# Kernel tuning notes

Hardware: AMD Instinct MI355X
Metric: run time of the kernel (lower is better)

Reference implementation:

```python
import jax, jax.numpy as jnp
import numpy as np
import math

B, T, D, H = 2, 2048, 1024, 16
DH = D // H


def setup_inputs() -> dict:
    key = jax.random.key(0)
    k1, k2, k3 = jax.random.split(key, 3)
    scale_in = 1.0 / math.sqrt(D)
    x = jax.random.normal(k1, (B, T, D), dtype=jnp.float32)
    w_qkv = jax.random.normal(k2, (D, 3 * D), dtype=jnp.float32) * scale_in
    b_qkv = jnp.zeros((3 * D,), dtype=jnp.float32)
    w_out = jax.random.normal(k3, (D, D), dtype=jnp.float32) * scale_in
    b_out = jnp.zeros((D,), dtype=jnp.float32)
    return {"x": x, "w_qkv": w_qkv, "b_qkv": b_qkv, "w_out": w_out, "b_out": b_out}


def reference(x, w_qkv, b_qkv, w_out, b_out):
    # Fused QKV projection: [B,T,3D]
    qkv = x @ w_qkv + b_qkv
    q, k, v = jnp.split(qkv, 3, axis=-1)
    # [B,H,T,DH]
    q = q.reshape(B, T, H, DH).transpose(0, 2, 1, 3)
    k = k.reshape(B, T, H, DH).transpose(0, 2, 1, 3)
    v = v.reshape(B, T, H, DH).transpose(0, 2, 1, 3)
    # scores: [B,H,T,T]
    scores = jnp.einsum('bhqd,bhkd->bhqk', q, k) / math.sqrt(DH)
    causal_mask = jnp.tril(jnp.ones((T, T), dtype=bool))
    scores = jnp.where(causal_mask, scores, -1e10)
    attn = jax.nn.softmax(scores, axis=-1)
    out = jnp.einsum('bhqk,bhkd->bhqd', attn, v)
    out = out.transpose(0, 2, 1, 3).reshape(B, T, D)
    return out @ w_out + b_out
```

## Files before the change

### kernel.cpp

```cpp
#include <hip/hip_runtime.h>
#include <hip/hip_bf16.h>
#include <stdint.h>

#define Bsz  2
#define Tseq 2048
#define Dmod 1024
#define Hn   16
#define DHd  64

typedef short bf16x8 __attribute__((ext_vector_type(8)));
typedef float f32x4 __attribute__((ext_vector_type(4)));

__device__ __forceinline__ float bf2f(unsigned short u) {
  union { unsigned int i; float f; } v; v.i = ((unsigned int)u) << 16; return v.f;
}
__device__ __forceinline__ unsigned short f2bf(float f) {
  union { float f; unsigned int i; } v; v.f = f;
  unsigned int r = (v.i + 0x7fffu + ((v.i >> 16) & 1u)) >> 16;
  return (unsigned short)r;
}
__device__ __forceinline__ unsigned int pk_bf16(float a, float b) {
  union { __hip_bfloat162 h; unsigned int u; } u2;
  u2.h = __float22bfloat162_rn(make_float2(a, b));
  return u2.u;
}
__device__ __forceinline__ void gl_lds16(const unsigned short* g, unsigned short* l) {
  __builtin_amdgcn_global_load_lds(
      (const __attribute__((address_space(1))) void*)g,
      (__attribute__((address_space(3))) void*)l, 16, 0, 0);
}

#define QSCALE 0.1803368801f

__global__ __launch_bounds__(256) void prep(const float* __restrict__ x,
                                            const float* __restrict__ w_qkv,
                                            const float* __restrict__ w_out,
                                            unsigned short* __restrict__ xb,
                                            unsigned short* __restrict__ wqkvT,
                                            unsigned short* __restrict__ woutT) {
  __shared__ unsigned short tile[64][65];
  const int blk = blockIdx.x;
  if (blk < 2048) {
    int idx = blk * 2048 + threadIdx.x * 8;
    float4 a = *(const float4*)&x[idx];
    float4 b = *(const float4*)&x[idx + 4];
    unsigned short o[8];
    o[0] = f2bf(a.x); o[1] = f2bf(a.y); o[2] = f2bf(a.z); o[3] = f2bf(a.w);
    o[4] = f2bf(b.x); o[5] = f2bf(b.y); o[6] = f2bf(b.z); o[7] = f2bf(b.w);
    *(uint4*)&xb[idx] = *(const uint4*)o;
    return;
  }
  const float* in;
  unsigned short* out;
  int K = 1024, N, k0, n0;
  if (blk < 2048 + 768) {
    int t = blk - 2048;
    in = w_qkv; out = wqkvT; N = 3072;
    n0 = (t % 48) * 64; k0 = (t / 48) * 64;
  } else {
    int t = blk - 2816;
    in = w_out; out = woutT; N = 1024;
    n0 = (t % 16) * 64; k0 = (t / 16) * 64;
  }
  for (int i = threadIdx.x; i < 4096; i += 256) {
    int r = i >> 6, c = i & 63;
    tile[r][c] = f2bf(in[(size_t)(k0 + r) * N + n0 + c]);
  }
  __syncthreads();
  for (int i = threadIdx.x; i < 4096; i += 256) {
    int r = i >> 6, c = i & 63;
    out[(size_t)(n0 + r) * K + k0 + c] = tile[c][r];
  }
}

template<int MT, int NT>
__global__ __launch_bounds__(256) void gemm_bt(const unsigned short* __restrict__ A,
                                               const unsigned short* __restrict__ Bt,
                                               const float* __restrict__ bias,
                                               int M, int N, int K, int mode,
                                               float* __restrict__ outF,
                                               unsigned short* __restrict__ out0,
                                               unsigned short* __restrict__ out1,
                                               unsigned short* __restrict__ out2) {
  constexpr int IT = MT / 32;
  constexpr int JT = NT / 32;
  constexpr int AP = MT / 64;
  constexpr int BP = NT / 64;
  __shared__ unsigned short As[2][MT * 32];
  __shared__ unsigned short Bs[2][NT * 32];
  const int tid  = threadIdx.x;
  const int lane = tid & 63;
  const int w    = tid >> 6;
  const int m0   = blockIdx.x * MT;
  const int n0   = blockIdx.y * NT;
  const int wr   = (w >> 1) * (MT / 2);
  const int wc   = (w & 1) * (NT / 2);

  f32x4 acc[IT][JT];
  for (int i = 0; i < IT; i++)
    for (int j = 0; j < JT; j++)
      for (int v = 0; v < 4; v++) acc[i][j][v] = 0.0f;

  const int l16  = lane & 15;
  const int g    = lane >> 4;
  const int fkey = (l16 & 3) ^ ((l16 >> 2) & 3);

  const int csw = (((lane & 3) ^ ((lane >> 2) & 3) ^ ((lane >> 4) & 3)) & 3) * 8;
  const unsigned short* ga[AP];
  const unsigned short* gb[BP];
  unsigned short* la[2][AP];
  unsigned short* lb[2][BP];
#pragma unroll
  for (int p = 0; p < AP; p++) {
    int r = (MT / 4) * w + 16 * p + (lane >> 2);
    ga[p] = A + (size_t)(m0 + r) * K + csw;
    la[0][p] = &As[0][((MT / 4) * w + 16 * p) * 32];
    la[1][p] = &As[1][((MT / 4) * w + 16 * p) * 32];
  }
#pragma unroll
  for (int p = 0; p < BP; p++) {
    int r = (NT / 4) * w + 16 * p + (lane >> 2);
    gb[p] = Bt + (size_t)(n0 + r) * K + csw;
    lb[0][p] = &Bs[0][((NT / 4) * w + 16 * p) * 32];
    lb[1][p] = &Bs[1][((NT / 4) * w + 16 * p) * 32];
  }

#pragma unroll
  for (int p = 0; p < AP; p++) gl_lds16(ga[p], la[0][p]);
#pragma unroll
  for (int p = 0; p < BP; p++) gl_lds16(gb[p], lb[0][p]);
  __syncthreads();

  for (int kt = 0; kt < K; kt += 32) {
    const int cur = (kt >> 5) & 1, nxt = cur ^ 1;
    if (kt + 32 < K) {
#pragma unroll
      for (int p = 0; p < AP; p++) gl_lds16(ga[p] + kt + 32, la[nxt][p]);
#pragma unroll
      for (int p = 0; p < BP; p++) gl_lds16(gb[p] + kt + 32, lb[nxt][p]);
    }
    bf16x8 af[IT], bf[JT];
#pragma unroll
    for (int i = 0; i < IT; i++)
      af[i] = *(const bf16x8*)&As[cur][(wr + i * 16 + l16) * 32 + ((g ^ fkey) * 8)];
#pragma unroll
    for (int j = 0; j < JT; j++)
      bf[j] = *(const bf16x8*)&Bs[cur][(wc + j * 16 + l16) * 32 + ((g ^ fkey) * 8)];
#pragma unroll
    for (int i = 0; i < IT; i++)
#pragma unroll
      for (int j = 0; j < JT; j++)
        acc[i][j] = __builtin_amdgcn_mfma_f32_16x16x32_bf16(af[i], bf[j], acc[i][j], 0, 0, 0);
    __syncthreads();
  }

  const int q4 = g * 4;
#pragma unroll
  for (int i = 0; i < IT; i++)
#pragma unroll
    for (int j = 0; j < JT; j++) {
      const int mbase = m0 + wr + i * 16 + q4;
      const int n = n0 + wc + j * 16 + l16;
      float vals[4];
#pragma unroll
      for (int v = 0; v < 4; v++) vals[v] = acc[i][j][v] + bias[n];
      if (mode == 1) {
#pragma unroll
        for (int v = 0; v < 4; v++)
          outF[(size_t)(mbase + v) * N + n] = vals[v];
      } else {
        const int which = n >> 10;
        const int rem = n & 1023;
        const int h = rem >> 6, dd = rem & 63;
        const int b = mbase >> 11, t = mbase & 2047;
        if (which == 2) {
          uint2 uu;
          uu.x = pk_bf16(vals[0], vals[1]);
          uu.y = pk_bf16(vals[2], vals[3]);
          *(uint2*)&out2[((size_t)((b * Hn + h) * DHd + dd)) * Tseq + t] = uu;
        } else if (which == 0) {
#pragma unroll
          for (int v = 0; v < 4; v++)
            out0[(size_t)((b * Hn + h) * Tseq + t + v) * DHd + dd] = f2bf(vals[v] * QSCALE);
        } else {
#pragma unroll
          for (int v = 0; v < 4; v++)
            out1[(size_t)((b * Hn + h) * Tseq + t + v) * DHd + dd] = f2bf(vals[v]);
        }
      }
    }
}

__global__ __launch_bounds__(256, 4) void attn_mfma(const unsigned short* __restrict__ Qb,
                                                    const unsigned short* __restrict__ Kb,
                                                    const unsigned short* __restrict__ Vtg,
                                                    unsigned short* __restrict__ O) {
  __shared__ unsigned short Ks[2][64 * 64];
  __shared__ unsigned short Vs[2][64 * 64];
  __shared__ unsigned short Ps[4][16 * 64];

  const int tid  = threadIdx.x;
  const int lane = tid & 63;
  const int w    = tid >> 6;
  const int g    = lane >> 4;
  const int l16  = lane & 15;
  const int bh   = blockIdx.x;
  const int tile = (int)gridDim.y - 1 - (int)blockIdx.y;
  const int q0w  = tile * 64 + w * 16;

  const unsigned short* Qp = Qb  + (size_t)bh * Tseq * DHd;
  const unsigned short* Kp = Kb  + (size_t)bh * Tseq * DHd;
  const unsigned short* Vp = Vtg + (size_t)bh * DHd * Tseq;

  bf16x8 qf[2];
#pragma unroll
  for (int ks = 0; ks < 2; ks++)
    qf[ks] = *(const bf16x8*)&Qp[(size_t)(q0w + l16) * DHd + ks * 32 + g * 8];

  f32x4 Oacc[4];
#pragma unroll
  for (int dt = 0; dt < 4; dt++)
#pragma unroll
    for (int v = 0; v < 4; v++) Oacc[dt][v] = 0.f;

  float lpart = 0.f;
  unsigned short* Pw = Ps[w];
  const int swz = l16 & 7;

  const int csw = (((lane & 7) ^ (lane >> 3)) & 7) * 8;
  const unsigned short* KgB = Kp + (size_t)(16 * w + (lane >> 3)) * DHd + csw;
  const unsigned short* VgB = Vp + (size_t)(16 * w + (lane >> 3)) * Tseq + csw;
  unsigned short* KsW[2] = { &Ks[0][16 * w * 64], &Ks[1][16 * w * 64] };
  unsigned short* VsW[2] = { &Vs[0][16 * w * 64], &Vs[1][16 * w * 64] };

  gl_lds16(KgB,             KsW[0]);
  gl_lds16(KgB + 8 * DHd,   KsW[0] + 8 * 64);
  gl_lds16(VgB,             VsW[0]);
  gl_lds16(VgB + 8 * Tseq,  VsW[0] + 8 * 64);
  __syncthreads();

  for (int c = 0; c <= tile; c++) {
    const int cur = c & 1, nxt = cur ^ 1;
    if (c < tile) {
      const size_t ko = (size_t)(c + 1) * 64 * DHd;
      const int    vo = (c + 1) * 64;
      gl_lds16(KgB + ko,            KsW[nxt]);
      gl_lds16(KgB + ko + 8 * DHd,  KsW[nxt] + 8 * 64);
      gl_lds16(VgB + vo,            VsW[nxt]);
      gl_lds16(VgB + vo + 8 * Tseq, VsW[nxt] + 8 * 64);
    }

    f32x4 st[4];
#pragma unroll
    for (int mt = 0; mt < 4; mt++)
#pragma unroll
      for (int v = 0; v < 4; v++) st[mt][v] = 0.f;
#pragma unroll
    for (int ks = 0; ks < 2; ks++) {
      bf16x8 kf[4];
#pragma unroll
      for (int mt = 0; mt < 4; mt++)
        kf[mt] = *(const bf16x8*)&Ks[cur][(16 * mt + l16) * 64 + (((ks * 4 + g) ^ swz) * 8)];
#pragma unroll
      for (int mt = 0; mt < 4; mt++)
        st[mt] = __builtin_amdgcn_mfma_f32_16x16x32_bf16(kf[mt], qf[ks], st[mt], 0, 0, 0);
    }

    if (c == tile) {
      const int qg = q0w + l16;
#pragma unroll
      for (int mt = 0; mt < 4; mt++)
#pragma unroll
        for (int v = 0; v < 4; v++)
          if ((c * 64 + 16 * mt + 4 * g + v) > qg) st[mt][v] = -1e30f;
    }
#pragma unroll
    for (int mt = 0; mt < 4; mt++) {
      float p[4];
#pragma unroll
      for (int v = 0; v < 4; v++) { p[v] = __builtin_exp2f(st[mt][v]); lpart += p[v]; }
      uint2 uu;
      uu.x = pk_bf16(p[0], p[1]);
      uu.y = pk_bf16(p[2], p[3]);
      *(uint2*)&Pw[l16 * 64 + (((2 * mt + (g >> 1)) ^ swz) << 3) + 4 * (g & 1)] = uu;
    }

#pragma unroll
    for (int ks = 0; ks < 2; ks++) {
      bf16x8 pf = *(const bf16x8*)&Pw[l16 * 64 + (((4 * ks + g) ^ swz) * 8)];
      bf16x8 vf[4];
#pragma unroll
      for (int dt = 0; dt < 4; dt++)
        vf[dt] = *(const bf16x8*)&Vs[cur][(16 * dt + l16) * 64 + (((4 * ks + g) ^ swz) * 8)];
#pragma unroll
      for (int dt = 0; dt < 4; dt++)
        Oacc[dt] = __builtin_amdgcn_mfma_f32_16x16x32_bf16(pf, vf[dt], Oacc[dt], 0, 0, 0);
    }

    __syncthreads();
  }

  float lrow = lpart;
  lrow += __shfl_xor(lrow, 16);
  lrow += __shfl_xor(lrow, 32);
  const float l0 = __shfl(lrow, 4 * g + 0);
  const float l1 = __shfl(lrow, 4 * g + 1);
  const float l2 = __shfl(lrow, 4 * g + 2);
  const float l3 = __shfl(lrow, 4 * g + 3);
  const float i0 = 1.f / l0, i1 = 1.f / l1, i2 = 1.f / l2, i3 = 1.f / l3;
  const int b = bh >> 4, h = bh & 15;
#pragma unroll
  for (int dt = 0; dt < 4; dt++) {
    const int d = h * DHd + 16 * dt + l16;
    const size_t r0 = (size_t)(b * Tseq + q0w + 4 * g) * Dmod + d;
    O[r0]            = f2bf(Oacc[dt][0] * i0);
    O[r0 + Dmod]     = f2bf(Oacc[dt][1] * i1);
    O[r0 + 2 * Dmod] = f2bf(Oacc[dt][2] * i2);
    O[r0 + 3 * Dmod] = f2bf(Oacc[dt][3] * i3);
  }
}

extern "C" void kernel_launch(void* const* d_in, const int* in_sizes, int n_in,
                              void* d_out, int out_size, void* d_ws, size_t ws_size,
                              hipStream_t stream) {
  (void)in_sizes; (void)n_in; (void)out_size; (void)ws_size;
  const float* x     = (const float*)d_in[0];
  const float* w_qkv = (const float*)d_in[1];
  const float* b_qkv = (const float*)d_in[2];
  const float* w_out = (const float*)d_in[3];
  const float* b_out = (const float*)d_in[4];
  float* out = (float*)d_out;

  unsigned short* ws    = (unsigned short*)d_ws;
  unsigned short* xb    = ws;
  unsigned short* wqkvT = xb    + (size_t)4194304;
  unsigned short* woutT = wqkvT + (size_t)3072 * 1024;
  unsigned short* Qb    = woutT + (size_t)1024 * 1024;
  unsigned short* Kb    = Qb + (size_t)4194304;
  unsigned short* Vt    = Kb + (size_t)4194304;
  unsigned short* Ob    = xb;

  prep<<<3072, 256, 0, stream>>>(x, w_qkv, w_out, xb, wqkvT, woutT);
  gemm_bt<128, 128><<<dim3(32, 24), 256, 0, stream>>>(xb, wqkvT, b_qkv, 4096, 3072, 1024, 0,
                                                      nullptr, Qb, Kb, Vt);
  attn_mfma<<<dim3(32, 32), 256, 0, stream>>>(Qb, Kb, Vt, Ob);
  gemm_bt<128, 128><<<dim3(32, 8), 256, 0, stream>>>(Ob, woutT, b_out, 4096, 1024, 1024, 1,
                                                     out, nullptr, nullptr, nullptr);
}
```

Baseline: 178.7 us.

## Use two-wave attention blocks with 32 query rows per wave; smaller output GEMM tiles

```diff
diff --git a/kernel.cpp b/kernel.cpp
--- a/kernel.cpp
+++ b/kernel.cpp
@@ -191,13 +191,13 @@
     }
 }
 
-__global__ __launch_bounds__(256, 4) void attn_mfma(const unsigned short* __restrict__ Qb,
+__global__ __launch_bounds__(128, 2) void attn_mfma(const unsigned short* __restrict__ Qb,
                                                     const unsigned short* __restrict__ Kb,
                                                     const unsigned short* __restrict__ Vtg,
                                                     unsigned short* __restrict__ O) {
   __shared__ unsigned short Ks[2][64 * 64];
   __shared__ unsigned short Vs[2][64 * 64];
-  __shared__ unsigned short Ps[4][16 * 64];
+  __shared__ unsigned short Ps[2][32 * 64];
 
   const int tid  = threadIdx.x;
   const int lane = tid & 63;
@@ -206,37 +206,43 @@
   const int l16  = lane & 15;
   const int bh   = blockIdx.x;
   const int tile = (int)gridDim.y - 1 - (int)blockIdx.y;
-  const int q0w  = tile * 64 + w * 16;
+  const int q0w  = tile * 64 + w * 32;
 
   const unsigned short* Qp = Qb  + (size_t)bh * Tseq * DHd;
   const unsigned short* Kp = Kb  + (size_t)bh * Tseq * DHd;
   const unsigned short* Vp = Vtg + (size_t)bh * DHd * Tseq;
 
-  bf16x8 qf[2];
-#pragma unroll
-  for (int ks = 0; ks < 2; ks++)
-    qf[ks] = *(const bf16x8*)&Qp[(size_t)(q0w + l16) * DHd + ks * 32 + g * 8];
-
-  f32x4 Oacc[4];
-#pragma unroll
-  for (int dt = 0; dt < 4; dt++)
-#pragma unroll
-    for (int v = 0; v < 4; v++) Oacc[dt][v] = 0.f;
-
-  float lpart = 0.f;
+  bf16x8 qf[2][2];
+#pragma unroll
+  for (int qq = 0; qq < 2; qq++)
+#pragma unroll
+    for (int ks = 0; ks < 2; ks++)
+      qf[qq][ks] = *(const bf16x8*)&Qp[(size_t)(q0w + qq * 16 + l16) * DHd + ks * 32 + g * 8];
+
+  f32x4 Oacc[2][4];
+#pragma unroll
+  for (int qq = 0; qq < 2; qq++)
+#pragma unroll
+    for (int dt = 0; dt < 4; dt++)
+#pragma unroll
+      for (int v = 0; v < 4; v++) Oacc[qq][dt][v] = 0.f;
+
+  const f32x4 FZ = {0.f, 0.f, 0.f, 0.f};
+  float lpart[2] = {0.f, 0.f};
   unsigned short* Pw = Ps[w];
   const int swz = l16 & 7;
 
   const int csw = (((lane & 7) ^ (lane >> 3)) & 7) * 8;
-  const unsigned short* KgB = Kp + (size_t)(16 * w + (lane >> 3)) * DHd + csw;
-  const unsigned short* VgB = Vp + (size_t)(16 * w + (lane >> 3)) * Tseq + csw;
-  unsigned short* KsW[2] = { &Ks[0][16 * w * 64], &Ks[1][16 * w * 64] };
-  unsigned short* VsW[2] = { &Vs[0][16 * w * 64], &Vs[1][16 * w * 64] };
-
-  gl_lds16(KgB,             KsW[0]);
-  gl_lds16(KgB + 8 * DHd,   KsW[0] + 8 * 64);
-  gl_lds16(VgB,             VsW[0]);
-  gl_lds16(VgB + 8 * Tseq,  VsW[0] + 8 * 64);
+  const unsigned short* KgB = Kp + (size_t)(32 * w + (lane >> 3)) * DHd + csw;
+  const unsigned short* VgB = Vp + (size_t)(32 * w + (lane >> 3)) * Tseq + csw;
+  unsigned short* KsW[2] = { &Ks[0][32 * w * 64], &Ks[1][32 * w * 64] };
+  unsigned short* VsW[2] = { &Vs[0][32 * w * 64], &Vs[1][32 * w * 64] };
+
+#pragma unroll
+  for (int r = 0; r < 4; r++) {
+    gl_lds16(KgB + r * 8 * DHd,  KsW[0] + r * 8 * 64);
+    gl_lds16(VgB + r * 8 * Tseq, VsW[0] + r * 8 * 64);
+  }
   __syncthreads();
 
   for (int c = 0; c <= tile; c++) {
@@ -244,79 +250,101 @@
     if (c < tile) {
       const size_t ko = (size_t)(c + 1) * 64 * DHd;
       const int    vo = (c + 1) * 64;
-      gl_lds16(KgB + ko,            KsW[nxt]);
-      gl_lds16(KgB + ko + 8 * DHd,  KsW[nxt] + 8 * 64);
-      gl_lds16(VgB + vo,            VsW[nxt]);
-      gl_lds16(VgB + vo + 8 * Tseq, VsW[nxt] + 8 * 64);
-    }
-
-    f32x4 st[4];
-#pragma unroll
-    for (int mt = 0; mt < 4; mt++)
-#pragma unroll
-      for (int v = 0; v < 4; v++) st[mt][v] = 0.f;
+#pragma unroll
+      for (int r = 0; r < 4; r++) {
+        gl_lds16(KgB + ko + r * 8 * DHd,  KsW[nxt] + r * 8 * 64);
+        gl_lds16(VgB + vo + r * 8 * Tseq, VsW[nxt] + r * 8 * 64);
+      }
+    }
+
+    f32x4 st[2][4];
+    {
+      bf16x8 kf[4];
+#pragma unroll
+      for (int mt = 0; mt < 4; mt++)
+        kf[mt] = *(const bf16x8*)&Ks[cur][(16 * mt + l16) * 64 + ((g ^ swz) * 8)];
+#pragma unroll
+      for (int qq = 0; qq < 2; qq++)
+#pragma unroll
+        for (int mt = 0; mt < 4; mt++)
+          st[qq][mt] = __builtin_amdgcn_mfma_f32_16x16x32_bf16(kf[mt], qf[qq][0], FZ, 0, 0, 0);
+    }
+    {
+      bf16x8 kf[4];
+#pragma unroll
+      for (int mt = 0; mt < 4; mt++)
+        kf[mt] = *(const bf16x8*)&Ks[cur][(16 * mt + l16) * 64 + (((4 + g) ^ swz) * 8)];
+#pragma unroll
+      for (int qq = 0; qq < 2; qq++)
+#pragma unroll
+        for (int mt = 0; mt < 4; mt++)
+          st[qq][mt] = __builtin_amdgcn_mfma_f32_16x16x32_bf16(kf[mt], qf[qq][1], st[qq][mt], 0, 0, 0);
+    }
+
+    if (c == tile) {
+#pragma unroll
+      for (int qq = 0; qq < 2; qq++) {
+        const int qg = q0w + qq * 16 + l16;
+#pragma unroll
+        for (int mt = 0; mt < 4; mt++)
+#pragma unroll
+          for (int v = 0; v < 4; v++)
+            if ((c * 64 + 16 * mt + 4 * g + v) > qg) st[qq][mt][v] = -1e30f;
+      }
+    }
+
+#pragma unroll
+    for (int qq = 0; qq < 2; qq++)
+#pragma unroll
+      for (int mt = 0; mt < 4; mt++) {
+        float p[4];
+#pragma unroll
+        for (int v = 0; v < 4; v++) { p[v] = __builtin_exp2f(st[qq][mt][v]); lpart[qq] += p[v]; }
+        uint2 uu;
+        uu.x = pk_bf16(p[0], p[1]);
+        uu.y = pk_bf16(p[2], p[3]);
+        *(uint2*)&Pw[(qq * 16 + l16) * 64 + (((2 * mt + (g >> 1)) ^ swz) << 3) + 4 * (g & 1)] = uu;
+      }
+
 #pragma unroll
     for (int ks = 0; ks < 2; ks++) {
-      bf16x8 kf[4];
-#pragma unroll
-      for (int mt = 0; mt < 4; mt++)
-        kf[mt] = *(const bf16x8*)&Ks[cur][(16 * mt + l16) * 64 + (((ks * 4 + g) ^ swz) * 8)];
-#pragma unroll
-      for (int mt = 0; mt < 4; mt++)
-        st[mt] = __builtin_amdgcn_mfma_f32_16x16x32_bf16(kf[mt], qf[ks], st[mt], 0, 0, 0);
-    }
-
-    if (c == tile) {
-      const int qg = q0w + l16;
-#pragma unroll
-      for (int mt = 0; mt < 4; mt++)
-#pragma unroll
-        for (int v = 0; v < 4; v++)
-          if ((c * 64 + 16 * mt + 4 * g + v) > qg) st[mt][v] = -1e30f;
-    }
-#pragma unroll
-    for (int mt = 0; mt < 4; mt++) {
-      float p[4];
-#pragma unroll
-      for (int v = 0; v < 4; v++) { p[v] = __builtin_exp2f(st[mt][v]); lpart += p[v]; }
-      uint2 uu;
-      uu.x = pk_bf16(p[0], p[1]);
-      uu.y = pk_bf16(p[2], p[3]);
-      *(uint2*)&Pw[l16 * 64 + (((2 * mt + (g >> 1)) ^ swz) << 3) + 4 * (g & 1)] = uu;
-    }
-
-#pragma unroll
-    for (int ks = 0; ks < 2; ks++) {
-      bf16x8 pf = *(const bf16x8*)&Pw[l16 * 64 + (((4 * ks + g) ^ swz) * 8)];
+      bf16x8 pf0 = *(const bf16x8*)&Pw[l16 * 64 + (((4 * ks + g) ^ swz) * 8)];
+      bf16x8 pf1 = *(const bf16x8*)&Pw[(16 + l16) * 64 + (((4 * ks + g) ^ swz) * 8)];
       bf16x8 vf[4];
 #pragma unroll
       for (int dt = 0; dt < 4; dt++)
         vf[dt] = *(const bf16x8*)&Vs[cur][(16 * dt + l16) * 64 + (((4 * ks + g) ^ swz) * 8)];
 #pragma unroll
       for (int dt = 0; dt < 4; dt++)
-        Oacc[dt] = __builtin_amdgcn_mfma_f32_16x16x32_bf16(pf, vf[dt], Oacc[dt], 0, 0, 0);
+        Oacc[0][dt] = __builtin_amdgcn_mfma_f32_16x16x32_bf16(pf0, vf[dt], Oacc[0][dt], 0, 0, 0);
+#pragma unroll
+      for (int dt = 0; dt < 4; dt++)
+        Oacc[1][dt] = __builtin_amdgcn_mfma_f32_16x16x32_bf16(pf1, vf[dt], Oacc[1][dt], 0, 0, 0);
     }
 
     __syncthreads();
   }
 
-  float lrow = lpart;
-  lrow += __shfl_xor(lrow, 16);
-  lrow += __shfl_xor(lrow, 32);
-  const float l0 = __shfl(lrow, 4 * g + 0);
-  const float l1 = __shfl(lrow, 4 * g + 1);
-  const float l2 = __shfl(lrow, 4 * g + 2);
-  const float l3 = __shfl(lrow, 4 * g + 3);
-  const float i0 = 1.f / l0, i1 = 1.f / l1, i2 = 1.f / l2, i3 = 1.f / l3;
   const int b = bh >> 4, h = bh & 15;
 #pragma unroll
-  for (int dt = 0; dt < 4; dt++) {
-    const int d = h * DHd + 16 * dt + l16;
-    const size_t r0 = (size_t)(b * Tseq + q0w + 4 * g) * Dmod + d;
-    O[r0]            = f2bf(Oacc[dt][0] * i0);
-    O[r0 + Dmod]     = f2bf(Oacc[dt][1] * i1);
-    O[r0 + 2 * Dmod] = f2bf(Oacc[dt][2] * i2);
-    O[r0 + 3 * Dmod] = f2bf(Oacc[dt][3] * i3);
+  for (int qq = 0; qq < 2; qq++) {
+    float lrow = lpart[qq];
+    lrow += __shfl_xor(lrow, 16);
+    lrow += __shfl_xor(lrow, 32);
+    const float l0 = __shfl(lrow, 4 * g + 0);
+    const float l1 = __shfl(lrow, 4 * g + 1);
+    const float l2 = __shfl(lrow, 4 * g + 2);
+    const float l3 = __shfl(lrow, 4 * g + 3);
+    const float i0 = 1.f / l0, i1 = 1.f / l1, i2 = 1.f / l2, i3 = 1.f / l3;
+#pragma unroll
+    for (int dt = 0; dt < 4; dt++) {
+      const int d = h * DHd + 16 * dt + l16;
+      const size_t r0 = (size_t)(b * Tseq + q0w + qq * 16 + 4 * g) * Dmod + d;
+      O[r0]            = f2bf(Oacc[qq][dt][0] * i0);
+      O[r0 + Dmod]     = f2bf(Oacc[qq][dt][1] * i1);
+      O[r0 + 2 * Dmod] = f2bf(Oacc[qq][dt][2] * i2);
+      O[r0 + 3 * Dmod] = f2bf(Oacc[qq][dt][3] * i3);
+    }
   }
 }
 
@@ -343,7 +371,7 @@
   prep<<<3072, 256, 0, stream>>>(x, w_qkv, w_out, xb, wqkvT, woutT);
   gemm_bt<128, 128><<<dim3(32, 24), 256, 0, stream>>>(xb, wqkvT, b_qkv, 4096, 3072, 1024, 0,
                                                       nullptr, Qb, Kb, Vt);
-  attn_mfma<<<dim3(32, 32), 256, 0, stream>>>(Qb, Kb, Vt, Ob);
-  gemm_bt<128, 128><<<dim3(32, 8), 256, 0, stream>>>(Ob, woutT, b_out, 4096, 1024, 1024, 1,
-                                                     out, nullptr, nullptr, nullptr);
-}
+  attn_mfma<<<dim3(32, 32), 128, 0, stream>>>(Qb, Kb, Vt, Ob);
+  gemm_bt<64, 64><<<dim3(64, 16), 256, 0, stream>>>(Ob, woutT, b_out, 4096, 1024, 1024, 1,
+                                                    out, nullptr, nullptr, nullptr);
+}
```

Measured after the change: 187.7 us. 5.1% more time.

## Keep softmax probabilities in registers by permuting V layout; retile output GEMM

Applied to the files above, without the earlier changes.

```diff
diff --git a/kernel.cpp b/kernel.cpp
--- a/kernel.cpp
+++ b/kernel.cpp
@@ -177,7 +177,8 @@
           uint2 uu;
           uu.x = pk_bf16(vals[0], vals[1]);
           uu.y = pk_bf16(vals[2], vals[3]);
-          *(uint2*)&out2[((size_t)((b * Hn + h) * DHd + dd)) * Tseq + t] = uu;
+          const int t2 = (t & ~63) | (t & 32) | (((t >> 2) & 3) << 3) | (((t >> 4) & 1) << 2);
+          *(uint2*)&out2[((size_t)((b * Hn + h) * DHd + dd)) * Tseq + t2] = uu;
         } else if (which == 0) {
 #pragma unroll
           for (int v = 0; v < 4; v++)
@@ -197,7 +198,6 @@
                                                     unsigned short* __restrict__ O) {
   __shared__ unsigned short Ks[2][64 * 64];
   __shared__ unsigned short Vs[2][64 * 64];
-  __shared__ unsigned short Ps[4][16 * 64];
 
   const int tid  = threadIdx.x;
   const int lane = tid & 63;
@@ -223,8 +223,8 @@
 #pragma unroll
     for (int v = 0; v < 4; v++) Oacc[dt][v] = 0.f;
 
+  const f32x4 FZ = {0.f, 0.f, 0.f, 0.f};
   float lpart = 0.f;
-  unsigned short* Pw = Ps[w];
   const int swz = l16 & 7;
 
   const int csw = (((lane & 7) ^ (lane >> 3)) & 7) * 8;
@@ -251,19 +251,23 @@
     }
 
     f32x4 st[4];
-#pragma unroll
-    for (int mt = 0; mt < 4; mt++)
-#pragma unroll
-      for (int v = 0; v < 4; v++) st[mt][v] = 0.f;
-#pragma unroll
-    for (int ks = 0; ks < 2; ks++) {
+    {
       bf16x8 kf[4];
 #pragma unroll
       for (int mt = 0; mt < 4; mt++)
-        kf[mt] = *(const bf16x8*)&Ks[cur][(16 * mt + l16) * 64 + (((ks * 4 + g) ^ swz) * 8)];
-#pragma unroll
-      for (int mt = 0; mt < 4; mt++)
-        st[mt] = __builtin_amdgcn_mfma_f32_16x16x32_bf16(kf[mt], qf[ks], st[mt], 0, 0, 0);
+        kf[mt] = *(const bf16x8*)&Ks[cur][(16 * mt + l16) * 64 + ((g ^ swz) * 8)];
+#pragma unroll
+      for (int mt = 0; mt < 4; mt++)
+        st[mt] = __builtin_amdgcn_mfma_f32_16x16x32_bf16(kf[mt], qf[0], FZ, 0, 0, 0);
+    }
+    {
+      bf16x8 kf[4];
+#pragma unroll
+      for (int mt = 0; mt < 4; mt++)
+        kf[mt] = *(const bf16x8*)&Ks[cur][(16 * mt + l16) * 64 + (((4 + g) ^ swz) * 8)];
+#pragma unroll
+      for (int mt = 0; mt < 4; mt++)
+        st[mt] = __builtin_amdgcn_mfma_f32_16x16x32_bf16(kf[mt], qf[1], st[mt], 0, 0, 0);
     }
 
     if (c == tile) {
@@ -274,20 +278,23 @@
         for (int v = 0; v < 4; v++)
           if ((c * 64 + 16 * mt + 4 * g + v) > qg) st[mt][v] = -1e30f;
     }
+
+    unsigned int pw[2][4];
 #pragma unroll
     for (int mt = 0; mt < 4; mt++) {
       float p[4];
 #pragma unroll
       for (int v = 0; v < 4; v++) { p[v] = __builtin_exp2f(st[mt][v]); lpart += p[v]; }
-      uint2 uu;
-      uu.x = pk_bf16(p[0], p[1]);
-      uu.y = pk_bf16(p[2], p[3]);
-      *(uint2*)&Pw[l16 * 64 + (((2 * mt + (g >> 1)) ^ swz) << 3) + 4 * (g & 1)] = uu;
+      pw[mt >> 1][(mt & 1) * 2 + 0] = pk_bf16(p[0], p[1]);
+      pw[mt >> 1][(mt & 1) * 2 + 1] = pk_bf16(p[2], p[3]);
     }
 
 #pragma unroll
     for (int ks = 0; ks < 2; ks++) {
-      bf16x8 pf = *(const bf16x8*)&Pw[l16 * 64 + (((4 * ks + g) ^ swz) * 8)];
+      union { unsigned int u[4]; bf16x8 v8; } pu;
+#pragma unroll
+      for (int m = 0; m < 4; m++) pu.u[m] = pw[ks][m];
+      const bf16x8 pf = pu.v8;
       bf16x8 vf[4];
 #pragma unroll
       for (int dt = 0; dt < 4; dt++)
@@ -344,6 +351,6 @@
   gemm_bt<128, 128><<<dim3(32, 24), 256, 0, stream>>>(xb, wqkvT, b_qkv, 4096, 3072, 1024, 0,
                                                       nullptr, Qb, Kb, Vt);
   attn_mfma<<<dim3(32, 32), 256, 0, stream>>>(Qb, Kb, Vt, Ob);
-  gemm_bt<128, 128><<<dim3(32, 8), 256, 0, stream>>>(Ob, woutT, b_out, 4096, 1024, 1024, 1,
-                                                     out, nullptr, nullptr, nullptr);
-}
+  gemm_bt<64, 64><<<dim3(64, 16), 256, 0, stream>>>(Ob, woutT, b_out, 4096, 1024, 1024, 1,
+                                                    out, nullptr, nullptr, nullptr);
+}
```

After: 174.6 us. -2.3%, faster.
